# Optimization experiments

Measured on AMD Instinct MI355X. Metric: run time of the kernel, lower is better.

Reference implementation:

```python
import jax, jax.numpy as jnp
import numpy as np

N_NODES = 100000
N_EDGES = 1600000
HIDDEN = 128
IN_FEAT = 7
N_CLASSES = 2
N_GRAPHS = 512


def _glorot(key, shape):
    lim = float(np.sqrt(6.0 / (shape[0] + shape[1])))
    return jax.random.uniform(key, shape, jnp.float32, -lim, lim)


def setup_inputs() -> dict:
    key = jax.random.key(0)
    ks = jax.random.split(key, 8)
    x = jax.random.normal(ks[0], (N_NODES, IN_FEAT), jnp.float32)
    edge_index = jax.random.randint(ks[1], (2, N_EDGES), 0, N_NODES, jnp.int32)
    batch_data = jnp.sort(jax.random.randint(ks[2], (N_NODES,), 0, N_GRAPHS, jnp.int32))
    return {
        "x": x,
        "edge_index": edge_index,
        "batch_data": batch_data,
        "W1": _glorot(ks[3], (IN_FEAT, HIDDEN)),
        "b1": jnp.zeros((HIDDEN,), jnp.float32),
        "W2": _glorot(ks[4], (HIDDEN, HIDDEN)),
        "b2": jnp.zeros((HIDDEN,), jnp.float32),
        "W3": _glorot(ks[5], (HIDDEN, HIDDEN)),
        "b3": jnp.zeros((HIDDEN,), jnp.float32),
        "Wl": _glorot(ks[6], (HIDDEN, N_CLASSES)),
        "bl": jnp.zeros((N_CLASSES,), jnp.float32),
    }


def reference(x, edge_index, batch_data, W1, b1, W2, b2, W3, b3, Wl, bl):
    n = x.shape[0]
    loops = jnp.arange(n, dtype=edge_index.dtype)
    src = jnp.concatenate([edge_index[0], loops])  # [E+N]
    dst = jnp.concatenate([edge_index[1], loops])
    # GCN symmetric normalization with self-loops (PyG gcn_norm default)
    deg = jax.ops.segment_sum(jnp.ones_like(dst, dtype=x.dtype), dst, num_segments=n)
    dis = jax.lax.rsqrt(deg)  # deg >= 1 thanks to self-loops
    norm = (dis[src] * dis[dst])[:, None]  # [E+N, 1]

    def gcn_relu(h, W, b):
        hw = h @ W                                  # [N, H] linear first (PyG GCNConv)
        msg = hw[src] * norm                        # gather + edge-normalize
        agg = jax.ops.segment_sum(msg, dst, num_segments=n)  # scatter-add
        return jax.nn.relu(agg + b)

    h = gcn_relu(x, W1, b1)
    h = gcn_relu(h, W2, b2)
    h = gcn_relu(h, W3, b3)
    pooled = jax.ops.segment_max(h, batch_data, num_segments=N_GRAPHS)  # [G, H]
    return pooled @ Wl + bl
```

## Files before the change

kernel.cpp:

```cpp
#include <hip/hip_runtime.h>
#include <hip/hip_fp16.h>

#define N_NODES 100000
#define N_EDGES 1600000
#define HID 128
#define N_GRAPHS 512
#define NBK 196
#define SEG 8192

typedef _Float16 f16x8 __attribute__((ext_vector_type(8)));
typedef float f32x4 __attribute__((ext_vector_type(4)));


__global__ void k_bhist(const int* __restrict__ dst, int e, int* __restrict__ bkcnt) {
    __shared__ int l[NBK];
    int tid = threadIdx.x;
    for (int i = tid; i < NBK; i += 256) l[i] = 0;
    __syncthreads();
    int base = blockIdx.x * SEG;
    int m = min(SEG, e - base);
    for (int i = tid; i < m; i += 256) atomicAdd(&l[dst[base + i] >> 9], 1);
    __syncthreads();
    for (int b = tid; b < NBK; b += 256)
        if (l[b]) atomicAdd(&bkcnt[b], l[b]);
}

__global__ void k_bscan(const int* __restrict__ bkcnt, int* __restrict__ bkoff,
                        int* __restrict__ bcur, int e) {
    __shared__ int s[256];
    int t = threadIdx.x;
    int v = (t < NBK) ? bkcnt[t] : 0;
    s[t] = v;
    __syncthreads();
    for (int off = 1; off < 256; off <<= 1) {
        int u = (t >= off) ? s[t - off] : 0;
        __syncthreads();
        s[t] += u;
        __syncthreads();
    }
    int excl = s[t] - v;
    if (t < NBK) { bkoff[t] = excl; bcur[t] = excl; }
    if (t == NBK - 1) bkoff[NBK] = excl + v;
}

__launch_bounds__(256) __global__
void k_passA(const int* __restrict__ ei, int* __restrict__ bcur,
             unsigned* __restrict__ pk, int e) {
    __shared__ int lcnt[NBK];
    __shared__ int lbase[NBK];
    int tid = threadIdx.x;
    int base = blockIdx.x * SEG;
    for (int i = tid; i < NBK; i += 256) lcnt[i] = 0;
    __syncthreads();
    int m = min(SEG, e - base);
    for (int i = tid; i < m; i += 256) {
        int d = ei[N_EDGES + base + i];
        atomicAdd(&lcnt[d >> 9], 1);
    }
    __syncthreads();
    for (int b = tid; b < NBK; b += 256)
        lbase[b] = lcnt[b] ? atomicAdd(&bcur[b], lcnt[b]) : 0;
    __syncthreads();
    for (int i = tid; i < m; i += 256) {
        int s = ei[base + i];
        int d = ei[N_EDGES + base + i];
        int pos = atomicAdd(&lbase[d >> 9], 1);
        pk[pos] = ((unsigned)s << 9) | (unsigned)(d & 511);
    }
}

__launch_bounds__(256) __global__
void k_passB(const unsigned* __restrict__ pk, const int* __restrict__ bkoff,
             int* __restrict__ rowptr, float* __restrict__ dis, float* __restrict__ dinv,
             int* __restrict__ csrc, int n, int e) {
    __shared__ int lcnt[512];
    __shared__ int lofs[512];
    __shared__ int sw[256];
    int b = blockIdx.x;
    int tid = threadIdx.x;
    int db0 = b * 512;
    int nd = min(512, n - db0);
    int pbeg = bkoff[b];
    int pend = bkoff[b + 1];
    lcnt[tid] = 0;
    lcnt[tid + 256] = 0;
    __syncthreads();
    for (int i = pbeg + tid; i < pend; i += 256) atomicAdd(&lcnt[pk[i] & 511], 1);
    __syncthreads();
    for (int j = tid; j < nd; j += 256) {
        float d = (float)(lcnt[j] + 1);
        dis[db0 + j] = rsqrtf(d);
        dinv[db0 + j] = 1.0f / d;
    }
    int a0 = lcnt[2 * tid];
    int a1 = lcnt[2 * tid + 1];
    int v = a0 + a1;
    sw[tid] = v;
    __syncthreads();
    for (int off = 1; off < 256; off <<= 1) {
        int u = (tid >= off) ? sw[tid - off] : 0;
        __syncthreads();
        sw[tid] += u;
        __syncthreads();
    }
    int excl = sw[tid] - v;
    lofs[2 * tid] = excl;
    lofs[2 * tid + 1] = excl + a0;
    __syncthreads();
    for (int j = tid; j < nd; j += 256) rowptr[db0 + j] = pbeg + lofs[j];
    if (db0 + nd == n && tid == 0) rowptr[n] = e;
    for (int j = tid; j < 512; j += 256) lcnt[j] = pbeg + lofs[j];
    __syncthreads();
    for (int i = pbeg + tid; i < pend; i += 256) {
        unsigned w = pk[i];
        int pos = atomicAdd(&lcnt[w & 511], 1);
        csrc[pos] = (int)(w >> 9);
    }
}


__global__ void k_linear1(const float* __restrict__ x, const float* __restrict__ W1,
                          __half* __restrict__ hw, int n) {
    __shared__ float W1s[7 * 128];
    int tid = threadIdx.x;
    for (int i = tid; i < 7 * 128; i += 256) W1s[i] = W1[i];
    __syncthreads();
    int node = blockIdx.x * 2 + (tid >> 7);
    if (node >= n) return;
    int c = tid & 127;
    const float* xr = x + (size_t)node * 7;
    float acc = 0.f;
#pragma unroll
    for (int k = 0; k < 7; ++k) acc += xr[k] * W1s[k * 128 + c];
    hw[(size_t)node * 128 + c] = __float2half_rn(acc);
}


__device__ __forceinline__ void acc8(uint2 p, float w, float4& a) {
    float2 lo = __half22float2(*(__half2*)&p.x);
    float2 hi = __half22float2(*(__half2*)&p.y);
    a.x += lo.x * w; a.y += lo.y * w; a.z += hi.x * w; a.w += hi.y * w;
}

__launch_bounds__(256) __global__
void k_gather(const int* __restrict__ rowptr, const int* __restrict__ csrc,
              const float* __restrict__ dis, const float* __restrict__ dinv,
              const uint2* __restrict__ hwv, uint2* __restrict__ aggv, int n) {
    int wid = blockIdx.x * 4 + (threadIdx.x >> 6);
    int lane = threadIdx.x & 63;
    int sub = lane >> 5;
    int c = lane & 31;
    int node = wid * 2 + sub;
    if (node >= n) return;

    int beg = rowptr[node];
    int end = rowptr[node + 1];
    int deg = end - beg;
    float dd = dis[node];
    float di = dinv[node];

    int sidx = 0;
    float wsc = 0.f;
    if (c < deg) {
        sidx = csrc[beg + c];
        wsc = dis[sidx];
    }

    int mown = deg < 32 ? deg : 32;
    int m = max(__shfl(mown, 0), __shfl(mown, 32));
    int sub32 = sub << 5;

    float4 a = make_float4(0.f, 0.f, 0.f, 0.f);
    int j = 0;
    for (; j + 3 < m; j += 4) {
        int s0 = __shfl(sidx, sub32 + j);     float w0 = __shfl(wsc, sub32 + j);
        int s1 = __shfl(sidx, sub32 + j + 1); float w1 = __shfl(wsc, sub32 + j + 1);
        int s2 = __shfl(sidx, sub32 + j + 2); float w2 = __shfl(wsc, sub32 + j + 2);
        int s3 = __shfl(sidx, sub32 + j + 3); float w3 = __shfl(wsc, sub32 + j + 3);
        uint2 p0 = hwv[(size_t)s0 * 32 + c];
        uint2 p1 = hwv[(size_t)s1 * 32 + c];
        uint2 p2 = hwv[(size_t)s2 * 32 + c];
        uint2 p3 = hwv[(size_t)s3 * 32 + c];
        acc8(p0, w0, a); acc8(p1, w1, a); acc8(p2, w2, a); acc8(p3, w3, a);
    }
    for (; j < m; ++j) {
        int s0 = __shfl(sidx, sub32 + j);
        float w0 = __shfl(wsc, sub32 + j);
        uint2 p0 = hwv[(size_t)s0 * 32 + c];
        acc8(p0, w0, a);
    }
    for (int jj = beg + 32; jj < end; ++jj) {
        int s0 = csrc[jj];
        float w0 = dis[s0];
        uint2 p0 = hwv[(size_t)s0 * 32 + c];
        acc8(p0, w0, a);
    }

    uint2 ps = hwv[(size_t)node * 32 + c];
    float2 slo = __half22float2(*(__half2*)&ps.x);
    float2 shi = __half22float2(*(__half2*)&ps.y);
    float4 r;
    r.x = slo.x * di + dd * a.x;
    r.y = slo.y * di + dd * a.y;
    r.z = shi.x * di + dd * a.z;
    r.w = shi.y * di + dd * a.w;
    __half2 lo = __floats2half2_rn(r.x, r.y);
    __half2 hi = __floats2half2_rn(r.z, r.w);
    uint2 o;
    o.x = *(unsigned*)&lo;
    o.y = *(unsigned*)&hi;
    aggv[(size_t)node * 32 + c] = o;
}


__device__ __forceinline__ int swz(int row, int kByte) {
    return row * 256 + (kByte ^ ((row & 7) << 4));
}

__launch_bounds__(256) __global__
void k_gemm_mfma(const __half* __restrict__ aggin, const float* __restrict__ b,
                 const float* __restrict__ W, __half* __restrict__ hwout, int n) {
    __shared__ __align__(16) _Float16 Wt[128 * 128];
    __shared__ __align__(16) _Float16 As[64 * 128];
    int tid = threadIdx.x;

    for (int i = tid; i < 128 * 128; i += 256) {
        int k = i >> 7;
        int nn = i & 127;
        *(_Float16*)((char*)Wt + swz(nn, k * 2)) = (_Float16)W[i];
    }

    int row = tid >> 2;
    int q = tid & 3;
    int wv = tid >> 6;
    int lane = tid & 63;
    int lo16 = lane & 15;
    int hi4 = lane >> 4;

    for (int t = 0; t < 2; ++t) {
        if (t) __syncthreads();
        int grow = blockIdx.x * 128 + t * 64 + row;
#pragma unroll
        for (int j = 0; j < 4; ++j) {
            int c0 = q * 32 + j * 8;
            uint4 pk = make_uint4(0u, 0u, 0u, 0u);
            if (grow < n) {
                uint4 p = *(const uint4*)(aggin + (size_t)grow * 128 + c0);
                float4 bA = *(const float4*)(b + c0);
                float4 bB = *(const float4*)(b + c0 + 4);
                float2 t0 = __half22float2(*(const __half2*)&p.x);
                float2 t1 = __half22float2(*(const __half2*)&p.y);
                float2 t2 = __half22float2(*(const __half2*)&p.z);
                float2 t3 = __half22float2(*(const __half2*)&p.w);
                __half2 h0 = __floats2half2_rn(fmaxf(t0.x + bA.x, 0.f), fmaxf(t0.y + bA.y, 0.f));
                __half2 h1 = __floats2half2_rn(fmaxf(t1.x + bA.z, 0.f), fmaxf(t1.y + bA.w, 0.f));
                __half2 h2 = __floats2half2_rn(fmaxf(t2.x + bB.x, 0.f), fmaxf(t2.y + bB.y, 0.f));
                __half2 h3 = __floats2half2_rn(fmaxf(t3.x + bB.z, 0.f), fmaxf(t3.y + bB.w, 0.f));
                pk.x = *(unsigned*)&h0; pk.y = *(unsigned*)&h1;
                pk.z = *(unsigned*)&h2; pk.w = *(unsigned*)&h3;
            }
            *(uint4*)((char*)As + swz(row, c0 * 2)) = pk;
        }
        __syncthreads();

        f32x4 acc[8];
#pragma unroll
        for (int nt = 0; nt < 8; ++nt) acc[nt] = (f32x4){0.f, 0.f, 0.f, 0.f};

        const char* Ab = (const char*)As;
        const char* Bb = (const char*)Wt;
#pragma unroll
        for (int kt = 0; kt < 4; ++kt) {
            int kByte = kt * 64 + hi4 * 16;
            f16x8 af = *(const f16x8*)(Ab + swz(wv * 16 + lo16, kByte));
#pragma unroll
            for (int nt = 0; nt < 8; ++nt) {
                f16x8 bf = *(const f16x8*)(Bb + swz(nt * 16 + lo16, kByte));
                acc[nt] = __builtin_amdgcn_mfma_f32_16x16x32_f16(af, bf, acc[nt], 0, 0, 0);
            }
        }

        int rbase = blockIdx.x * 128 + t * 64 + wv * 16 + hi4 * 4;
#pragma unroll
        for (int nt = 0; nt < 8; ++nt) {
#pragma unroll
            for (int r = 0; r < 4; ++r) {
                int node = rbase + r;
                if (node < n)
                    hwout[(size_t)node * 128 + nt * 16 + lo16] = __float2half_rn(acc[nt][r]);
            }
        }
    }
}


__global__ void k_pool_max(const __half* __restrict__ agg, const float* __restrict__ b,
                           const int* __restrict__ batch, unsigned* __restrict__ pooled, int n) {
    int idx = blockIdx.x * 256 + threadIdx.x;
    int node = idx >> 7;
    if (node >= n) return;
    int c = idx & 127;
    int g = batch[node];
    float v = __half2float(agg[(size_t)node * 128 + c]) + b[c];
    v = fmaxf(v, 0.f);
    atomicMax(&pooled[(size_t)g * 128 + c], __float_as_uint(v));
}


__global__ void k_final(const float* __restrict__ pooled, const float* __restrict__ Wl,
                        const float* __restrict__ bl, float* __restrict__ out) {
    int g = blockIdx.x;
    int t = threadIdx.x;
    float p0 = pooled[(size_t)g * 128 + t];
    float p1 = pooled[(size_t)g * 128 + t + 64];
    float a0 = p0 * Wl[t * 2 + 0] + p1 * Wl[(t + 64) * 2 + 0];
    float a1 = p0 * Wl[t * 2 + 1] + p1 * Wl[(t + 64) * 2 + 1];
#pragma unroll
    for (int off = 32; off > 0; off >>= 1) {
        a0 += __shfl_down(a0, off);
        a1 += __shfl_down(a1, off);
    }
    if (t == 0) {
        out[g * 2 + 0] = a0 + bl[0];
        out[g * 2 + 1] = a1 + bl[1];
    }
}


extern "C" void kernel_launch(void* const* d_in, const int* in_sizes, int n_in,
                              void* d_out, int out_size, void* d_ws, size_t ws_size,
                              hipStream_t stream) {
    const float* x  = (const float*)d_in[0];
    const int*   ei = (const int*)d_in[1];
    const int*   batch = (const int*)d_in[2];
    const float* W1 = (const float*)d_in[3];
    const float* b1 = (const float*)d_in[4];
    const float* W2 = (const float*)d_in[5];
    const float* b2 = (const float*)d_in[6];
    const float* W3 = (const float*)d_in[7];
    const float* b3 = (const float*)d_in[8];
    const float* Wl = (const float*)d_in[9];
    const float* bl = (const float*)d_in[10];
    float* out = (float*)d_out;

    const int N = N_NODES, E = N_EDGES;

    char* ws = (char*)d_ws;
    __half* bufA = (__half*)ws;
    __half* bufB = bufA + (size_t)N * 128;
    unsigned* pooled = (unsigned*)(bufB + (size_t)N * 128);
    float* dis  = (float*)(pooled + (size_t)N_GRAPHS * 128);
    float* dinv = dis + N;
    int*   rowptr = (int*)(dinv + N);
    int*   bkcnt  = rowptr + N + 2;
    int*   bkoff  = bkcnt + 256;
    int*   bcur   = bkoff + 256;
    int*   csrc   = bcur + 256;
    unsigned* pk  = (unsigned*)(csrc + E);

    hipMemsetAsync(bkcnt, 0, NBK * sizeof(int), stream);
    int nseg = (E + SEG - 1) / SEG;
    k_bhist<<<nseg, 256, 0, stream>>>(ei + E, E, bkcnt);
    k_bscan<<<1, 256, 0, stream>>>(bkcnt, bkoff, bcur, E);
    k_passA<<<nseg, 256, 0, stream>>>(ei, bcur, pk, E);
    k_passB<<<NBK, 256, 0, stream>>>(pk, bkoff, rowptr, dis, dinv, csrc, N, E);

    int ggrid = (N + 7) / 8;
    int mfma_grid = (N + 127) / 128;

    k_linear1<<<(N + 1) / 2, 256, 0, stream>>>(x, W1, bufA, N);
    k_gather<<<ggrid, 256, 0, stream>>>(rowptr, csrc, dis, dinv,
                                        (const uint2*)bufA, (uint2*)bufB, N);

    k_gemm_mfma<<<mfma_grid, 256, 0, stream>>>(bufB, b1, W2, bufA, N);
    k_gather<<<ggrid, 256, 0, stream>>>(rowptr, csrc, dis, dinv,
                                        (const uint2*)bufA, (uint2*)bufB, N);

    k_gemm_mfma<<<mfma_grid, 256, 0, stream>>>(bufB, b2, W3, bufA, N);
    k_gather<<<ggrid, 256, 0, stream>>>(rowptr, csrc, dis, dinv,
                                        (const uint2*)bufA, (uint2*)bufB, N);

    hipMemsetAsync(pooled, 0, (size_t)N_GRAPHS * 128 * sizeof(unsigned), stream);
    k_pool_max<<<(N * 128 + 255) / 256, 256, 0, stream>>>(bufB, b3, batch, pooled, N);

    k_final<<<N_GRAPHS, 64, 0, stream>>>((const float*)pooled, Wl, bl, out);
}
```

Baseline: 459.3 us.

## Aggregate raw 7-dim features before layer-1 linear and fuse last gather with pooling

```diff
diff --git a/kernel.cpp b/kernel.cpp
--- a/kernel.cpp
+++ b/kernel.cpp
@@ -119,20 +119,141 @@
 }
 
 
-__global__ void k_linear1(const float* __restrict__ x, const float* __restrict__ W1,
-                          __half* __restrict__ hw, int n) {
-    __shared__ float W1s[7 * 128];
+__global__ void k_padx(const float* __restrict__ x, float* __restrict__ x8, int n) {
+    int i = blockIdx.x * 256 + threadIdx.x;
+    if (i >= n * 8) return;
+    int node = i >> 3;
+    int k = i & 7;
+    x8[i] = (k < 7) ? x[node * 7 + k] : 0.f;
+}
+
+
+__launch_bounds__(256) __global__
+void k_gather7(const int* __restrict__ rowptr, const int* __restrict__ csrc,
+               const float* __restrict__ dis, const float* __restrict__ dinv,
+               const float2* __restrict__ x8v, float2* __restrict__ aggxv, int n) {
+    int idx = blockIdx.x * 256 + threadIdx.x;
+    int node = idx >> 2;
+    if (node >= n) return;
+    int qq = idx & 3;
+    int beg = rowptr[node];
+    int end = rowptr[node + 1];
+    float dd = dis[node];
+    float di = dinv[node];
+    float2 acc = make_float2(0.f, 0.f);
+    int j = beg;
+    for (; j + 1 < end; j += 2) {
+        int s0 = csrc[j];
+        int s1 = csrc[j + 1];
+        float w0 = dis[s0];
+        float w1 = dis[s1];
+        float2 v0 = x8v[(size_t)s0 * 4 + qq];
+        float2 v1 = x8v[(size_t)s1 * 4 + qq];
+        acc.x += v0.x * w0 + v1.x * w1;
+        acc.y += v0.y * w0 + v1.y * w1;
+    }
+    if (j < end) {
+        int s0 = csrc[j];
+        float w0 = dis[s0];
+        float2 v0 = x8v[(size_t)s0 * 4 + qq];
+        acc.x += v0.x * w0;
+        acc.y += v0.y * w0;
+    }
+    float2 ps = x8v[(size_t)node * 4 + qq];
+    float2 r;
+    r.x = ps.x * di + dd * acc.x;
+    r.y = ps.y * di + dd * acc.y;
+    aggxv[(size_t)node * 4 + qq] = r;
+}
+
+
+__device__ __forceinline__ int swz(int row, int kByte) {
+    return row * 256 + (kByte ^ ((row & 7) << 4));
+}
+
+__launch_bounds__(256) __global__
+void k_l12(const float2* __restrict__ aggxv, const float* __restrict__ b1,
+           const float* __restrict__ W1, const float* __restrict__ W2,
+           __half* __restrict__ hwout, int n) {
+    __shared__ __align__(16) _Float16 Wt[128 * 128];
+    __shared__ __align__(16) _Float16 As[64 * 128];
     int tid = threadIdx.x;
-    for (int i = tid; i < 7 * 128; i += 256) W1s[i] = W1[i];
-    __syncthreads();
-    int node = blockIdx.x * 2 + (tid >> 7);
-    if (node >= n) return;
-    int c = tid & 127;
-    const float* xr = x + (size_t)node * 7;
-    float acc = 0.f;
-#pragma unroll
-    for (int k = 0; k < 7; ++k) acc += xr[k] * W1s[k * 128 + c];
-    hw[(size_t)node * 128 + c] = __float2half_rn(acc);
+
+    for (int i = tid; i < 128 * 128; i += 256) {
+        int k = i >> 7;
+        int nn = i & 127;
+        *(_Float16*)((char*)Wt + swz(nn, k * 2)) = (_Float16)W2[i];
+    }
+
+    int rg = tid >> 5;
+    int c4 = tid & 31;
+    int col = c4 * 4;
+    float4 w1k[7];
+#pragma unroll
+    for (int k = 0; k < 7; ++k) w1k[k] = *(const float4*)(W1 + k * 128 + col);
+    float4 bb = *(const float4*)(b1 + col);
+
+    int wv = tid >> 6;
+    int lane = tid & 63;
+    int lo16 = lane & 15;
+    int hi4 = lane >> 4;
+
+    for (int t = 0; t < 2; ++t) {
+        if (t) __syncthreads();
+#pragma unroll
+        for (int rl = 0; rl < 8; ++rl) {
+            int row = rg * 8 + rl;
+            int grow = blockIdx.x * 128 + t * 64 + row;
+            uint2 pk2 = make_uint2(0u, 0u);
+            if (grow < n) {
+                float2 a0 = aggxv[(size_t)grow * 4 + 0];
+                float2 a1 = aggxv[(size_t)grow * 4 + 1];
+                float2 a2 = aggxv[(size_t)grow * 4 + 2];
+                float2 a3 = aggxv[(size_t)grow * 4 + 3];
+                float4 acc = bb;
+                acc.x += a0.x*w1k[0].x + a0.y*w1k[1].x + a1.x*w1k[2].x + a1.y*w1k[3].x
+                       + a2.x*w1k[4].x + a2.y*w1k[5].x + a3.x*w1k[6].x;
+                acc.y += a0.x*w1k[0].y + a0.y*w1k[1].y + a1.x*w1k[2].y + a1.y*w1k[3].y
+                       + a2.x*w1k[4].y + a2.y*w1k[5].y + a3.x*w1k[6].y;
+                acc.z += a0.x*w1k[0].z + a0.y*w1k[1].z + a1.x*w1k[2].z + a1.y*w1k[3].z
+                       + a2.x*w1k[4].z + a2.y*w1k[5].z + a3.x*w1k[6].z;
+                acc.w += a0.x*w1k[0].w + a0.y*w1k[1].w + a1.x*w1k[2].w + a1.y*w1k[3].w
+                       + a2.x*w1k[4].w + a2.y*w1k[5].w + a3.x*w1k[6].w;
+                __half2 h0 = __floats2half2_rn(fmaxf(acc.x, 0.f), fmaxf(acc.y, 0.f));
+                __half2 h1 = __floats2half2_rn(fmaxf(acc.z, 0.f), fmaxf(acc.w, 0.f));
+                pk2.x = *(unsigned*)&h0;
+                pk2.y = *(unsigned*)&h1;
+            }
+            *(uint2*)((char*)As + swz(row, c4 * 8)) = pk2;
+        }
+        __syncthreads();
+
+        f32x4 acc[8];
+#pragma unroll
+        for (int nt = 0; nt < 8; ++nt) acc[nt] = (f32x4){0.f, 0.f, 0.f, 0.f};
+        const char* Ab = (const char*)As;
+        const char* Bb = (const char*)Wt;
+#pragma unroll
+        for (int kt = 0; kt < 4; ++kt) {
+            int kByte = kt * 64 + hi4 * 16;
+            f16x8 af = *(const f16x8*)(Ab + swz(wv * 16 + lo16, kByte));
+#pragma unroll
+            for (int nt = 0; nt < 8; ++nt) {
+                f16x8 bf = *(const f16x8*)(Bb + swz(nt * 16 + lo16, kByte));
+                acc[nt] = __builtin_amdgcn_mfma_f32_16x16x32_f16(af, bf, acc[nt], 0, 0, 0);
+            }
+        }
+        int rbase = blockIdx.x * 128 + t * 64 + wv * 16 + hi4 * 4;
+#pragma unroll
+        for (int nt = 0; nt < 8; ++nt) {
+#pragma unroll
+            for (int r = 0; r < 4; ++r) {
+                int node = rbase + r;
+                if (node < n)
+                    hwout[(size_t)node * 128 + nt * 16 + lo16] = __float2half_rn(acc[nt][r]);
+            }
+        }
+    }
 }
 
 
@@ -172,16 +293,25 @@
 
     float4 a = make_float4(0.f, 0.f, 0.f, 0.f);
     int j = 0;
-    for (; j + 3 < m; j += 4) {
+    for (; j + 7 < m; j += 8) {
         int s0 = __shfl(sidx, sub32 + j);     float w0 = __shfl(wsc, sub32 + j);
         int s1 = __shfl(sidx, sub32 + j + 1); float w1 = __shfl(wsc, sub32 + j + 1);
         int s2 = __shfl(sidx, sub32 + j + 2); float w2 = __shfl(wsc, sub32 + j + 2);
         int s3 = __shfl(sidx, sub32 + j + 3); float w3 = __shfl(wsc, sub32 + j + 3);
+        int s4 = __shfl(sidx, sub32 + j + 4); float w4 = __shfl(wsc, sub32 + j + 4);
+        int s5 = __shfl(sidx, sub32 + j + 5); float w5 = __shfl(wsc, sub32 + j + 5);
+        int s6 = __shfl(sidx, sub32 + j + 6); float w6 = __shfl(wsc, sub32 + j + 6);
+        int s7 = __shfl(sidx, sub32 + j + 7); float w7 = __shfl(wsc, sub32 + j + 7);
         uint2 p0 = hwv[(size_t)s0 * 32 + c];
         uint2 p1 = hwv[(size_t)s1 * 32 + c];
         uint2 p2 = hwv[(size_t)s2 * 32 + c];
         uint2 p3 = hwv[(size_t)s3 * 32 + c];
+        uint2 p4 = hwv[(size_t)s4 * 32 + c];
+        uint2 p5 = hwv[(size_t)s5 * 32 + c];
+        uint2 p6 = hwv[(size_t)s6 * 32 + c];
+        uint2 p7 = hwv[(size_t)s7 * 32 + c];
         acc8(p0, w0, a); acc8(p1, w1, a); acc8(p2, w2, a); acc8(p3, w3, a);
+        acc8(p4, w4, a); acc8(p5, w5, a); acc8(p6, w6, a); acc8(p7, w7, a);
     }
     for (; j < m; ++j) {
         int s0 = __shfl(sidx, sub32 + j);
@@ -213,9 +343,87 @@
 }
 
 
-__device__ __forceinline__ int swz(int row, int kByte) {
-    return row * 256 + (kByte ^ ((row & 7) << 4));
-}
+__launch_bounds__(256) __global__
+void k_gatherpool(const int* __restrict__ rowptr, const int* __restrict__ csrc,
+                  const float* __restrict__ dis, const float* __restrict__ dinv,
+                  const uint2* __restrict__ hwv, const float* __restrict__ b3,
+                  const int* __restrict__ batch, unsigned* __restrict__ pooled, int n) {
+    int wid = blockIdx.x * 4 + (threadIdx.x >> 6);
+    int lane = threadIdx.x & 63;
+    int sub = lane >> 5;
+    int c = lane & 31;
+    int node = wid * 2 + sub;
+    if (node >= n) return;
+
+    int beg = rowptr[node];
+    int end = rowptr[node + 1];
+    int deg = end - beg;
+    float dd = dis[node];
+    float di = dinv[node];
+
+    int sidx = 0;
+    float wsc = 0.f;
+    if (c < deg) {
+        sidx = csrc[beg + c];
+        wsc = dis[sidx];
+    }
+
+    int mown = deg < 32 ? deg : 32;
+    int m = max(__shfl(mown, 0), __shfl(mown, 32));
+    int sub32 = sub << 5;
+
+    float4 a = make_float4(0.f, 0.f, 0.f, 0.f);
+    int j = 0;
+    for (; j + 7 < m; j += 8) {
+        int s0 = __shfl(sidx, sub32 + j);     float w0 = __shfl(wsc, sub32 + j);
+        int s1 = __shfl(sidx, sub32 + j + 1); float w1 = __shfl(wsc, sub32 + j + 1);
+        int s2 = __shfl(sidx, sub32 + j + 2); float w2 = __shfl(wsc, sub32 + j + 2);
+        int s3 = __shfl(sidx, sub32 + j + 3); float w3 = __shfl(wsc, sub32 + j + 3);
+        int s4 = __shfl(sidx, sub32 + j + 4); float w4 = __shfl(wsc, sub32 + j + 4);
+        int s5 = __shfl(sidx, sub32 + j + 5); float w5 = __shfl(wsc, sub32 + j + 5);
+        int s6 = __shfl(sidx, sub32 + j + 6); float w6 = __shfl(wsc, sub32 + j + 6);
+        int s7 = __shfl(sidx, sub32 + j + 7); float w7 = __shfl(wsc, sub32 + j + 7);
+        uint2 p0 = hwv[(size_t)s0 * 32 + c];
+        uint2 p1 = hwv[(size_t)s1 * 32 + c];
+        uint2 p2 = hwv[(size_t)s2 * 32 + c];
+        uint2 p3 = hwv[(size_t)s3 * 32 + c];
+        uint2 p4 = hwv[(size_t)s4 * 32 + c];
+        uint2 p5 = hwv[(size_t)s5 * 32 + c];
+        uint2 p6 = hwv[(size_t)s6 * 32 + c];
+        uint2 p7 = hwv[(size_t)s7 * 32 + c];
+        acc8(p0, w0, a); acc8(p1, w1, a); acc8(p2, w2, a); acc8(p3, w3, a);
+        acc8(p4, w4, a); acc8(p5, w5, a); acc8(p6, w6, a); acc8(p7, w7, a);
+    }
+    for (; j < m; ++j) {
+        int s0 = __shfl(sidx, sub32 + j);
+        float w0 = __shfl(wsc, sub32 + j);
+        uint2 p0 = hwv[(size_t)s0 * 32 + c];
+        acc8(p0, w0, a);
+    }
+    for (int jj = beg + 32; jj < end; ++jj) {
+        int s0 = csrc[jj];
+        float w0 = dis[s0];
+        uint2 p0 = hwv[(size_t)s0 * 32 + c];
+        acc8(p0, w0, a);
+    }
+
+    uint2 ps = hwv[(size_t)node * 32 + c];
+    float2 slo = __half22float2(*(__half2*)&ps.x);
+    float2 shi = __half22float2(*(__half2*)&ps.y);
+    float4 bb = *(const float4*)(b3 + c * 4);
+    float4 r;
+    r.x = fmaxf(slo.x * di + dd * a.x + bb.x, 0.f);
+    r.y = fmaxf(slo.y * di + dd * a.y + bb.y, 0.f);
+    r.z = fmaxf(shi.x * di + dd * a.z + bb.z, 0.f);
+    r.w = fmaxf(shi.y * di + dd * a.w + bb.w, 0.f);
+    int g = batch[node];
+    unsigned* pp = pooled + (size_t)g * 128 + c * 4;
+    atomicMax(pp + 0, __float_as_uint(r.x));
+    atomicMax(pp + 1, __float_as_uint(r.y));
+    atomicMax(pp + 2, __float_as_uint(r.z));
+    atomicMax(pp + 3, __float_as_uint(r.w));
+}
+
 
 __launch_bounds__(256) __global__
 void k_gemm_mfma(const __half* __restrict__ aggin, const float* __restrict__ b,
@@ -294,19 +502,6 @@
 }
 
 
-__global__ void k_pool_max(const __half* __restrict__ agg, const float* __restrict__ b,
-                           const int* __restrict__ batch, unsigned* __restrict__ pooled, int n) {
-    int idx = blockIdx.x * 256 + threadIdx.x;
-    int node = idx >> 7;
-    if (node >= n) return;
-    int c = idx & 127;
-    int g = batch[node];
-    float v = __half2float(agg[(size_t)node * 128 + c]) + b[c];
-    v = fmaxf(v, 0.f);
-    atomicMax(&pooled[(size_t)g * 128 + c], __float_as_uint(v));
-}
-
-
 __global__ void k_final(const float* __restrict__ pooled, const float* __restrict__ Wl,
                         const float* __restrict__ bl, float* __restrict__ out) {
     int g = blockIdx.x;
@@ -357,6 +552,8 @@
     int*   bcur   = bkoff + 256;
     int*   csrc   = bcur + 256;
     unsigned* pk  = (unsigned*)(csrc + E);
+    float* x8   = (float*)pk;
+    float* aggx = x8 + (size_t)N * 8;
 
     hipMemsetAsync(bkcnt, 0, NBK * sizeof(int), stream);
     int nseg = (E + SEG - 1) / SEG;
@@ -368,20 +565,18 @@
     int ggrid = (N + 7) / 8;
     int mfma_grid = (N + 127) / 128;
 
-    k_linear1<<<(N + 1) / 2, 256, 0, stream>>>(x, W1, bufA, N);
+    k_padx<<<(N * 8 + 255) / 256, 256, 0, stream>>>(x, x8, N);
+    k_gather7<<<(N * 4 + 255) / 256, 256, 0, stream>>>(rowptr, csrc, dis, dinv,
+                                                       (const float2*)x8, (float2*)aggx, N);
+    k_l12<<<mfma_grid, 256, 0, stream>>>((const float2*)aggx, b1, W1, W2, bufA, N);
+
     k_gather<<<ggrid, 256, 0, stream>>>(rowptr, csrc, dis, dinv,
                                         (const uint2*)bufA, (uint2*)bufB, N);
-
-    k_gemm_mfma<<<mfma_grid, 256, 0, stream>>>(bufB, b1, W2, bufA, N);
-    k_gather<<<ggrid, 256, 0, stream>>>(rowptr, csrc, dis, dinv,
-                                        (const uint2*)bufA, (uint2*)bufB, N);
-
     k_gemm_mfma<<<mfma_grid, 256, 0, stream>>>(bufB, b2, W3, bufA, N);
-    k_gather<<<ggrid, 256, 0, stream>>>(rowptr, csrc, dis, dinv,
-                                        (const uint2*)bufA, (uint2*)bufB, N);
 
     hipMemsetAsync(pooled, 0, (size_t)N_GRAPHS * 128 * sizeof(unsigned), stream);
-    k_pool_max<<<(N * 128 + 255) / 256, 256, 0, stream>>>(bufB, b3, batch, pooled, N);
+    k_gatherpool<<<ggrid, 256, 0, stream>>>(rowptr, csrc, dis, dinv,
+                                            (const uint2*)bufA, b3, batch, pooled, N);
 
     k_final<<<N_GRAPHS, 64, 0, stream>>>((const float*)pooled, Wl, bl, out);
 }
```

Result: slower. 483.5 us (+5.3%).
